# Kernel optimization log

Measured on AMD Instinct MI355X. Metric: run time of the kernel, lower is better.

The kernel has to match this reference:

```python
import jax, jax.numpy as jnp
import numpy as np

# Dimensions (decode path: seq_len == 1)
NS, SL = 32, 1            # num_seqs, query seq_len
NH, KVH, HS = 32, 8, 128  # query heads, kv heads, head size
QPK = NH // KVH           # queries per kv head (GQA)
X = 8                     # vLLM key-cache vectorization factor
NB, BS = 4096, 16         # num cache blocks, block_size
MB = 128                  # max blocks per sequence -> max_context_len = MB*BS = 2048
SCALE = 1.0 / float(np.sqrt(HS))


def setup_inputs() -> dict:
    key = jax.random.key(0)
    ks = jax.random.split(key, 6)
    query = jax.random.normal(ks[0], (NS, SL, NH * HS), jnp.float32)
    k_new = jax.random.normal(ks[1], (NS, SL, KVH * HS), jnp.float32)
    v_new = jax.random.normal(ks[2], (NS, SL, KVH * HS), jnp.float32)
    key_cache = jax.random.normal(ks[3], (NB, KVH, HS // X, BS, X), jnp.float32)
    value_cache = jax.random.normal(ks[4], (NB, KVH, HS, BS), jnp.float32)
    # disjoint block assignment: seq n owns blocks [n*MB, (n+1)*MB)
    block_tables = jnp.arange(NS * MB, dtype=jnp.int32).reshape(NS, MB)
    context_lens = jax.random.randint(ks[5], (NS,), 1, MB * BS + 1, jnp.int32)
    last = context_lens - 1  # position of the token being written this step
    slot_mapping = (block_tables[jnp.arange(NS), last // BS] * BS + last % BS)
    slot_mapping = slot_mapping.reshape(NS, SL).astype(jnp.int32)
    return dict(query=query, key=k_new, value=v_new, key_cache=key_cache,
                value_cache=value_cache, block_tables=block_tables,
                context_lens=context_lens, slot_mapping=slot_mapping)


def reference(query, key, value, key_cache, value_cache, block_tables,
              context_lens, slot_mapping):
    ns, sl, _ = query.shape
    q = query.reshape(ns * sl, NH, HS)
    k_new = key.reshape(ns * sl, KVH, HS)
    v_new = value.reshape(ns * sl, KVH, HS)
    slots = slot_mapping.reshape(-1)
    blk, off = slots // BS, slots % BS
    # reshape_and_cache: scatter new K/V into paged caches
    # key_cache[b, h, d, s, x] stores head-dim index d*X + x
    kc = key_cache.at[blk, :, :, off, :].set(k_new.reshape(-1, KVH, HS // X, X))
    vc = value_cache.at[blk, :, :, off].set(v_new)
    # reconstruct contiguous layout [NB, BS, KVH, HS]
    K = jnp.transpose(kc, (0, 3, 1, 2, 4)).reshape(NB, BS, KVH, HS)
    V = jnp.transpose(vc, (0, 3, 1, 2))
    # paged gather via block tables -> per-seq KV [ns, MB*BS, KVH, HS]
    Kg = K[block_tables].reshape(ns, MB * BS, KVH, HS)
    Vg = V[block_tables].reshape(ns, MB * BS, KVH, HS)
    # GQA attention: group query heads by kv head
    qr = q.reshape(ns, KVH, QPK, HS)
    scores = jnp.einsum('nkqd,nlkd->nkql', qr, Kg) * SCALE
    mask = jnp.arange(MB * BS)[None, :] < context_lens[:, None]  # [ns, L]
    scores = jnp.where(mask[:, None, None, :], scores, -jnp.inf)
    p = jax.nn.softmax(scores, axis=-1)
    out = jnp.einsum('nkql,nlkd->nkqd', p, Vg)
    return out.reshape(ns, sl, NH * HS)
```

## Files before the change

kernel.cpp:

```cpp
#include <hip/hip_runtime.h>
#include <math.h>

#define NSQ   32
#define NHQ   32
#define KVHN  8
#define HSZ   128
#define QPK   4
#define BSZ   16
#define MBL   128
#define LMAX  2048
#define SPLIT 256
#define NSPLIT (LMAX / SPLIT)
#define KSCALE 0.08838834764831843f

#define OPART_FLOATS (NSQ * KVHN * NSPLIT * QPK * HSZ)

__global__ __launch_bounds__(256) void pa_scatter(
    const float* __restrict__ key, const float* __restrict__ value,
    float* __restrict__ kc, float* __restrict__ vc,
    const int* __restrict__ slot_mapping)
{
    int seq  = blockIdx.x;
    int slot = slot_mapping[seq];
    int blk  = slot >> 4;
    int off  = slot & 15;
    for (int idx = threadIdx.x; idx < KVHN * HSZ; idx += 256) {
        int h  = idx >> 7;
        int d  = idx & 127;
        int d2 = d >> 3;
        int x  = d & 7;
        kc[(size_t)blk * 16384 + h * 2048 + d2 * 128 + off * 8 + x] = key[seq * (KVHN*HSZ) + idx];
        vc[(size_t)blk * 16384 + h * 2048 + d * 16 + off]           = value[seq * (KVHN*HSZ) + idx];
    }
}

__global__ __launch_bounds__(256) void pa_attn_split(
    const float* __restrict__ query,
    const float* __restrict__ kc,
    const float* __restrict__ vc,
    const int* __restrict__ block_tables,
    const int* __restrict__ context_lens,
    float* __restrict__ opart,
    float* __restrict__ ml)
{
    const int wg    = blockIdx.x;
    const int split = wg & (NSPLIT - 1);
    const int kvh   = (wg >> 3) & (KVHN - 1);
    const int seq   = wg >> 6;
    const int ctx   = context_lens[seq];
    const int start = split * SPLIT;
    if (start >= ctx) return;
    const int nvalid = min(SPLIT, ctx - start);

    __shared__ float4 q4[QPK][HSZ / 4];
    __shared__ float4 sc4[SPLIT];
    __shared__ float  vbuf[2 * BSZ][HSZ];
    __shared__ float  part[QPK][HSZ];
    __shared__ int    btab[SPLIT / BSZ];
    __shared__ float  redmax[4][QPK];
    __shared__ float  redsum[4][QPK];

    const int t = threadIdx.x;

    for (int i = t; i < QPK * (HSZ / 4); i += 256) {
        int h = i >> 5, dv = i & 31;
        const float* qp = query + seq * (NHQ*HSZ) + (kvh * QPK + h) * HSZ + dv * 4;
        q4[h][dv] = *(const float4*)qp;
    }
    if (t < SPLIT / BSZ) btab[t] = block_tables[seq * MBL + (start >> 4) + t];
    __syncthreads();

    const float* kp = kc + (size_t)btab[t >> 4] * 16384 + kvh * 2048 + (t & 15) * 8;
    float acc[QPK] = {0.f, 0.f, 0.f, 0.f};
    #pragma unroll
    for (int d2 = 0; d2 < 16; ++d2) {
        float4 k0 = *(const float4*)(kp + d2 * 128);
        float4 k1 = *(const float4*)(kp + d2 * 128 + 4);
        #pragma unroll
        for (int h = 0; h < QPK; ++h) {
            float4 q0 = q4[h][d2 * 2];
            float4 q1 = q4[h][d2 * 2 + 1];
            acc[h] += k0.x * q0.x + k0.y * q0.y + k0.z * q0.z + k0.w * q0.w
                    + k1.x * q1.x + k1.y * q1.y + k1.z * q1.z + k1.w * q1.w;
        }
    }
    const bool valid = (t < nvalid);
    float score[QPK];
    #pragma unroll
    for (int h = 0; h < QPK; ++h)
        score[h] = valid ? acc[h] * KSCALE : -INFINITY;

    float vmax[QPK];
    #pragma unroll
    for (int h = 0; h < QPK; ++h) {
        vmax[h] = score[h];
        #pragma unroll
        for (int off = 32; off > 0; off >>= 1)
            vmax[h] = fmaxf(vmax[h], __shfl_down(vmax[h], off));
    }
    const int wave = t >> 6, lane = t & 63;
    if (lane == 0) {
        #pragma unroll
        for (int h = 0; h < QPK; ++h) redmax[wave][h] = vmax[h];
    }
    __syncthreads();
    float mx[QPK];
    #pragma unroll
    for (int h = 0; h < QPK; ++h)
        mx[h] = fmaxf(fmaxf(redmax[0][h], redmax[1][h]),
                      fmaxf(redmax[2][h], redmax[3][h]));

    float e[QPK];
    #pragma unroll
    for (int h = 0; h < QPK; ++h)
        e[h] = valid ? __expf(score[h] - mx[h]) : 0.0f;
    sc4[t] = make_float4(e[0], e[1], e[2], e[3]);
    float lsum[QPK];
    #pragma unroll
    for (int h = 0; h < QPK; ++h) {
        lsum[h] = e[h];
        #pragma unroll
        for (int off = 32; off > 0; off >>= 1)
            lsum[h] += __shfl_down(lsum[h], off);
    }
    if (lane == 0) {
        #pragma unroll
        for (int h = 0; h < QPK; ++h) redsum[wave][h] = lsum[h];
    }
    __syncthreads();
    float lsumtot[QPK];
    #pragma unroll
    for (int h = 0; h < QPK; ++h)
        lsumtot[h] = redsum[0][h] + redsum[1][h] + redsum[2][h] + redsum[3][h];

    const int part_idx = (seq * KVHN + kvh) * NSPLIT + split;
    if (t < QPK) {
        ml[part_idx * QPK * 2 + t * 2 + 0] = mx[t];
        ml[part_idx * QPK * 2 + t * 2 + 1] = lsumtot[t];
    }

    const int d    = t & 127;
    const int half = t >> 7;
    float oacc[QPK] = {0.f, 0.f, 0.f, 0.f};
    const int nchunks = (nvalid + 31) >> 5;
    for (int c = 0; c < nchunks; ++c) {
        __syncthreads();
        {
            const int b    = half;
            const float* vptr = vc + (size_t)btab[2 * c + b] * 16384 + kvh * 2048 + d * 16;
            float4 a0 = *(const float4*)(vptr + 0);
            float4 a1 = *(const float4*)(vptr + 4);
            float4 a2 = *(const float4*)(vptr + 8);
            float4 a3 = *(const float4*)(vptr + 12);
            float* vb = &vbuf[b * BSZ][d];
            vb[0*HSZ]=a0.x; vb[1*HSZ]=a0.y; vb[2*HSZ]=a0.z; vb[3*HSZ]=a0.w;
            vb[4*HSZ]=a1.x; vb[5*HSZ]=a1.y; vb[6*HSZ]=a1.z; vb[7*HSZ]=a1.w;
            vb[8*HSZ]=a2.x; vb[9*HSZ]=a2.y; vb[10*HSZ]=a2.z; vb[11*HSZ]=a2.w;
            vb[12*HSZ]=a3.x; vb[13*HSZ]=a3.y; vb[14*HSZ]=a3.z; vb[15*HSZ]=a3.w;
        }
        __syncthreads();
        const int rbase = half * BSZ;
        #pragma unroll
        for (int s = 0; s < BSZ; ++s) {
            int row = rbase + s;
            float4 p = sc4[c * 32 + row];
            float  v = vbuf[row][d];
            oacc[0] += p.x * v; oacc[1] += p.y * v;
            oacc[2] += p.z * v; oacc[3] += p.w * v;
        }
    }

    __syncthreads();
    if (half == 1) {
        #pragma unroll
        for (int h = 0; h < QPK; ++h) part[h][d] = oacc[h];
    }
    __syncthreads();
    if (half == 0) {
        float* op = opart + (size_t)part_idx * QPK * HSZ;
        #pragma unroll
        for (int h = 0; h < QPK; ++h)
            op[h * HSZ + d] = oacc[h] + part[h][d];
    }
}

__global__ __launch_bounds__(256) void pa_combine(
    const float* __restrict__ opart,
    const float* __restrict__ ml,
    const int* __restrict__ context_lens,
    float* __restrict__ out)
{
    const int seq = blockIdx.x;
    const int t   = threadIdx.x;
    const int ctx = context_lens[seq];
    const int nact = (ctx + SPLIT - 1) / SPLIT;

    __shared__ float scale[KVHN][QPK][NSPLIT];
    __shared__ float invden[KVHN][QPK];

    if (t < KVHN * QPK) {
        int kvh = t >> 2, hh = t & 3;
        const float* mlp = ml + ((seq * KVHN + kvh) * NSPLIT) * QPK * 2 + hh * 2;
        float m = -INFINITY;
        for (int s = 0; s < nact; ++s)
            m = fmaxf(m, mlp[s * QPK * 2]);
        float den = 0.0f;
        for (int s = 0; s < nact; ++s) {
            float sc = __expf(mlp[s * QPK * 2] - m);
            scale[kvh][hh][s] = sc;
            den += sc * mlp[s * QPK * 2 + 1];
        }
        invden[kvh][hh] = 1.0f / den;
    }
    __syncthreads();

    for (int rep = 0; rep < NHQ * HSZ / 256; ++rep) {
        int idx = rep * 256 + t;
        int hq = idx >> 7, d = idx & 127;
        int kvh = hq >> 2, hh = hq & 3;
        const float* op = opart + ((size_t)(seq * KVHN + kvh) * NSPLIT) * QPK * HSZ + hh * HSZ + d;
        float num = 0.0f;
        for (int s = 0; s < nact; ++s)
            num += scale[kvh][hh][s] * op[s * QPK * HSZ];
        out[seq * (NHQ*HSZ) + idx] = num * invden[kvh][hh];
    }
}

extern "C" void kernel_launch(void* const* d_in, const int* in_sizes, int n_in,
                              void* d_out, int out_size, void* d_ws, size_t ws_size,
                              hipStream_t stream) {
    (void)in_sizes; (void)n_in; (void)ws_size; (void)out_size;
    const float* query        = (const float*)d_in[0];
    const float* key          = (const float*)d_in[1];
    const float* value        = (const float*)d_in[2];
    float*       key_cache    = (float*)d_in[3];
    float*       value_cache  = (float*)d_in[4];
    const int*   block_tables = (const int*)d_in[5];
    const int*   context_lens = (const int*)d_in[6];
    const int*   slot_mapping = (const int*)d_in[7];
    float*       out          = (float*)d_out;

    float* opart = (float*)d_ws;
    float* ml    = opart + OPART_FLOATS;

    hipLaunchKernelGGL(pa_scatter, dim3(NSQ), dim3(256), 0, stream,
                       key, value, key_cache, value_cache, slot_mapping);
    hipLaunchKernelGGL(pa_attn_split, dim3(NSQ * KVHN * NSPLIT), dim3(256), 0, stream,
                       query, key_cache, value_cache, block_tables, context_lens,
                       opart, ml);
    hipLaunchKernelGGL(pa_combine, dim3(NSQ), dim3(256), 0, stream,
                       opart, ml, context_lens, out);
}
```

Before: 517.9 us.

## Halve split size, drop LDS staging, and parallelize combine per kv head

Shrinks the context split from 256 to 128 tokens, so each workgroup uses 128 threads and the grid doubles. Query is read straight from global memory instead of being staged in LDS. The V path loads each cache block into registers per thread, which removes the shared V buffer, the per-chunk barriers and the two-half reduction. The grid is reordered split-major, and the combine kernel now runs one workgroup per (seq, kv head) instead of per sequence. The aim is more parallelism and fewer synchronizations, at the cost of more partials to combine and redundant query reads per thread.

```diff
diff --git a/kernel.cpp b/kernel.cpp
--- a/kernel.cpp
+++ b/kernel.cpp
@@ -9,7 +9,7 @@
 #define BSZ   16
 #define MBL   128
 #define LMAX  2048
-#define SPLIT 256
+#define SPLIT 128
 #define NSPLIT (LMAX / SPLIT)
 #define KSCALE 0.08838834764831843f
 
@@ -34,7 +34,7 @@
     }
 }
 
-__global__ __launch_bounds__(256) void pa_attn_split(
+__global__ __launch_bounds__(128) void pa_attn_split(
     const float* __restrict__ query,
     const float* __restrict__ kc,
     const float* __restrict__ vc,
@@ -44,45 +44,42 @@
     float* __restrict__ ml)
 {
     const int wg    = blockIdx.x;
-    const int split = wg & (NSPLIT - 1);
-    const int kvh   = (wg >> 3) & (KVHN - 1);
-    const int seq   = wg >> 6;
+    const int split = wg >> 8;
+    const int sk    = wg & 255;
+    const int seq   = sk >> 3;
+    const int kvh   = sk & 7;
     const int ctx   = context_lens[seq];
     const int start = split * SPLIT;
     if (start >= ctx) return;
     const int nvalid = min(SPLIT, ctx - start);
 
-    __shared__ float4 q4[QPK][HSZ / 4];
     __shared__ float4 sc4[SPLIT];
-    __shared__ float  vbuf[2 * BSZ][HSZ];
-    __shared__ float  part[QPK][HSZ];
-    __shared__ int    btab[SPLIT / BSZ];
-    __shared__ float  redmax[4][QPK];
-    __shared__ float  redsum[4][QPK];
+    __shared__ float  redmax[2][QPK];
+    __shared__ float  redsum[2][QPK];
 
     const int t = threadIdx.x;
 
-    for (int i = t; i < QPK * (HSZ / 4); i += 256) {
-        int h = i >> 5, dv = i & 31;
-        const float* qp = query + seq * (NHQ*HSZ) + (kvh * QPK + h) * HSZ + dv * 4;
-        q4[h][dv] = *(const float4*)qp;
-    }
-    if (t < SPLIT / BSZ) btab[t] = block_tables[seq * MBL + (start >> 4) + t];
-    __syncthreads();
-
-    const float* kp = kc + (size_t)btab[t >> 4] * 16384 + kvh * 2048 + (t & 15) * 8;
+    const int   blk = block_tables[seq * MBL + (start >> 4) + (t >> 4)];
+    const float* kp = kc + (size_t)blk * 16384 + kvh * 2048 + (t & 15) * 8;
+    const float4* qr0 = (const float4*)(query + seq * (NHQ*HSZ) + (kvh * QPK + 0) * HSZ);
+    const float4* qr1 = (const float4*)(query + seq * (NHQ*HSZ) + (kvh * QPK + 1) * HSZ);
+    const float4* qr2 = (const float4*)(query + seq * (NHQ*HSZ) + (kvh * QPK + 2) * HSZ);
+    const float4* qr3 = (const float4*)(query + seq * (NHQ*HSZ) + (kvh * QPK + 3) * HSZ);
+
     float acc[QPK] = {0.f, 0.f, 0.f, 0.f};
     #pragma unroll
     for (int d2 = 0; d2 < 16; ++d2) {
         float4 k0 = *(const float4*)(kp + d2 * 128);
         float4 k1 = *(const float4*)(kp + d2 * 128 + 4);
-        #pragma unroll
-        for (int h = 0; h < QPK; ++h) {
-            float4 q0 = q4[h][d2 * 2];
-            float4 q1 = q4[h][d2 * 2 + 1];
-            acc[h] += k0.x * q0.x + k0.y * q0.y + k0.z * q0.z + k0.w * q0.w
-                    + k1.x * q1.x + k1.y * q1.y + k1.z * q1.z + k1.w * q1.w;
-        }
+        float4 q;
+        q = qr0[d2*2];   acc[0] += k0.x*q.x + k0.y*q.y + k0.z*q.z + k0.w*q.w;
+        q = qr0[d2*2+1]; acc[0] += k1.x*q.x + k1.y*q.y + k1.z*q.z + k1.w*q.w;
+        q = qr1[d2*2];   acc[1] += k0.x*q.x + k0.y*q.y + k0.z*q.z + k0.w*q.w;
+        q = qr1[d2*2+1]; acc[1] += k1.x*q.x + k1.y*q.y + k1.z*q.z + k1.w*q.w;
+        q = qr2[d2*2];   acc[2] += k0.x*q.x + k0.y*q.y + k0.z*q.z + k0.w*q.w;
+        q = qr2[d2*2+1]; acc[2] += k1.x*q.x + k1.y*q.y + k1.z*q.z + k1.w*q.w;
+        q = qr3[d2*2];   acc[3] += k0.x*q.x + k0.y*q.y + k0.z*q.z + k0.w*q.w;
+        q = qr3[d2*2+1]; acc[3] += k1.x*q.x + k1.y*q.y + k1.z*q.z + k1.w*q.w;
     }
     const bool valid = (t < nvalid);
     float score[QPK];
@@ -107,8 +104,7 @@
     float mx[QPK];
     #pragma unroll
     for (int h = 0; h < QPK; ++h)
-        mx[h] = fmaxf(fmaxf(redmax[0][h], redmax[1][h]),
-                      fmaxf(redmax[2][h], redmax[3][h]));
+        mx[h] = fmaxf(redmax[0][h], redmax[1][h]);
 
     float e[QPK];
     #pragma unroll
@@ -128,101 +124,77 @@
         for (int h = 0; h < QPK; ++h) redsum[wave][h] = lsum[h];
     }
     __syncthreads();
-    float lsumtot[QPK];
-    #pragma unroll
-    for (int h = 0; h < QPK; ++h)
-        lsumtot[h] = redsum[0][h] + redsum[1][h] + redsum[2][h] + redsum[3][h];
 
     const int part_idx = (seq * KVHN + kvh) * NSPLIT + split;
     if (t < QPK) {
         ml[part_idx * QPK * 2 + t * 2 + 0] = mx[t];
-        ml[part_idx * QPK * 2 + t * 2 + 1] = lsumtot[t];
-    }
-
-    const int d    = t & 127;
-    const int half = t >> 7;
+        ml[part_idx * QPK * 2 + t * 2 + 1] = redsum[0][t] + redsum[1][t];
+    }
+
+    const int d = t;
     float oacc[QPK] = {0.f, 0.f, 0.f, 0.f};
-    const int nchunks = (nvalid + 31) >> 5;
-    for (int c = 0; c < nchunks; ++c) {
-        __syncthreads();
-        {
-            const int b    = half;
-            const float* vptr = vc + (size_t)btab[2 * c + b] * 16384 + kvh * 2048 + d * 16;
-            float4 a0 = *(const float4*)(vptr + 0);
-            float4 a1 = *(const float4*)(vptr + 4);
-            float4 a2 = *(const float4*)(vptr + 8);
-            float4 a3 = *(const float4*)(vptr + 12);
-            float* vb = &vbuf[b * BSZ][d];
-            vb[0*HSZ]=a0.x; vb[1*HSZ]=a0.y; vb[2*HSZ]=a0.z; vb[3*HSZ]=a0.w;
-            vb[4*HSZ]=a1.x; vb[5*HSZ]=a1.y; vb[6*HSZ]=a1.z; vb[7*HSZ]=a1.w;
-            vb[8*HSZ]=a2.x; vb[9*HSZ]=a2.y; vb[10*HSZ]=a2.z; vb[11*HSZ]=a2.w;
-            vb[12*HSZ]=a3.x; vb[13*HSZ]=a3.y; vb[14*HSZ]=a3.z; vb[15*HSZ]=a3.w;
+    const int nblk = (nvalid + 15) >> 4;
+    for (int bi = 0; bi < nblk; ++bi) {
+        const int vb = block_tables[seq * MBL + (start >> 4) + bi];
+        const float* vptr = vc + (size_t)vb * 16384 + kvh * 2048 + d * 16;
+        float4 a0 = *(const float4*)(vptr + 0);
+        float4 a1 = *(const float4*)(vptr + 4);
+        float4 a2 = *(const float4*)(vptr + 8);
+        float4 a3 = *(const float4*)(vptr + 12);
+        float v[16] = {a0.x,a0.y,a0.z,a0.w, a1.x,a1.y,a1.z,a1.w,
+                       a2.x,a2.y,a2.z,a2.w, a3.x,a3.y,a3.z,a3.w};
+        #pragma unroll
+        for (int s = 0; s < BSZ; ++s) {
+            float4 p = sc4[bi * BSZ + s];
+            oacc[0] += p.x * v[s]; oacc[1] += p.y * v[s];
+            oacc[2] += p.z * v[s]; oacc[3] += p.w * v[s];
         }
-        __syncthreads();
-        const int rbase = half * BSZ;
-        #pragma unroll
-        for (int s = 0; s < BSZ; ++s) {
-            int row = rbase + s;
-            float4 p = sc4[c * 32 + row];
-            float  v = vbuf[row][d];
-            oacc[0] += p.x * v; oacc[1] += p.y * v;
-            oacc[2] += p.z * v; oacc[3] += p.w * v;
-        }
-    }
-
-    __syncthreads();
-    if (half == 1) {
-        #pragma unroll
-        for (int h = 0; h < QPK; ++h) part[h][d] = oacc[h];
-    }
-    __syncthreads();
-    if (half == 0) {
-        float* op = opart + (size_t)part_idx * QPK * HSZ;
-        #pragma unroll
-        for (int h = 0; h < QPK; ++h)
-            op[h * HSZ + d] = oacc[h] + part[h][d];
-    }
-}
-
-__global__ __launch_bounds__(256) void pa_combine(
+    }
+
+    float* op = opart + (size_t)part_idx * QPK * HSZ;
+    #pragma unroll
+    for (int h = 0; h < QPK; ++h)
+        op[h * HSZ + d] = oacc[h];
+}
+
+__global__ __launch_bounds__(128) void pa_combine(
     const float* __restrict__ opart,
     const float* __restrict__ ml,
     const int* __restrict__ context_lens,
     float* __restrict__ out)
 {
-    const int seq = blockIdx.x;
+    const int seq = blockIdx.x >> 3;
+    const int kvh = blockIdx.x & 7;
     const int t   = threadIdx.x;
     const int ctx = context_lens[seq];
     const int nact = (ctx + SPLIT - 1) / SPLIT;
-
-    __shared__ float scale[KVHN][QPK][NSPLIT];
-    __shared__ float invden[KVHN][QPK];
-
-    if (t < KVHN * QPK) {
-        int kvh = t >> 2, hh = t & 3;
-        const float* mlp = ml + ((seq * KVHN + kvh) * NSPLIT) * QPK * 2 + hh * 2;
+    const int part0 = (seq * KVHN + kvh) * NSPLIT;
+
+    __shared__ float s_scale[QPK][NSPLIT];
+    __shared__ float s_inv[QPK];
+
+    if (t < QPK) {
+        const float* mlp = ml + part0 * QPK * 2 + t * 2;
         float m = -INFINITY;
         for (int s = 0; s < nact; ++s)
             m = fmaxf(m, mlp[s * QPK * 2]);
         float den = 0.0f;
         for (int s = 0; s < nact; ++s) {
             float sc = __expf(mlp[s * QPK * 2] - m);
-            scale[kvh][hh][s] = sc;
+            s_scale[t][s] = sc;
             den += sc * mlp[s * QPK * 2 + 1];
         }
-        invden[kvh][hh] = 1.0f / den;
+        s_inv[t] = 1.0f / den;
     }
     __syncthreads();
 
-    for (int rep = 0; rep < NHQ * HSZ / 256; ++rep) {
-        int idx = rep * 256 + t;
-        int hq = idx >> 7, d = idx & 127;
-        int kvh = hq >> 2, hh = hq & 3;
-        const float* op = opart + ((size_t)(seq * KVHN + kvh) * NSPLIT) * QPK * HSZ + hh * HSZ + d;
+    #pragma unroll
+    for (int h = 0; h < QPK; ++h) {
+        const float* op = opart + (size_t)part0 * QPK * HSZ + h * HSZ + t;
         float num = 0.0f;
         for (int s = 0; s < nact; ++s)
-            num += scale[kvh][hh][s] * op[s * QPK * HSZ];
-        out[seq * (NHQ*HSZ) + idx] = num * invden[kvh][hh];
+            num += s_scale[h][s] * op[(size_t)s * QPK * HSZ];
+        out[seq * (NHQ*HSZ) + (kvh * QPK + h) * HSZ + t] = num * s_inv[h];
     }
 }
 
@@ -245,9 +217,9 @@
 
     hipLaunchKernelGGL(pa_scatter, dim3(NSQ), dim3(256), 0, stream,
                        key, value, key_cache, value_cache, slot_mapping);
-    hipLaunchKernelGGL(pa_attn_split, dim3(NSQ * KVHN * NSPLIT), dim3(256), 0, stream,
+    hipLaunchKernelGGL(pa_attn_split, dim3(NSPLIT * NSQ * KVHN), dim3(SPLIT), 0, stream,
                        query, key_cache, value_cache, block_tables, context_lens,
                        opart, ml);
-    hipLaunchKernelGGL(pa_combine, dim3(NSQ), dim3(256), 0, stream,
+    hipLaunchKernelGGL(pa_combine, dim3(NSQ * KVHN), dim3(128), 0, stream,
                        opart, ml, context_lens, out);
 }
```

After: 496.1 us. -4.2%, faster.
